# Optimization experiments

Measured on AMD Instinct MI355X. Metric: run time of the kernel, lower is better.

## Reference

```python
import jax, jax.numpy as jnp
import numpy as np
import math

B, S, D, H = 2, 2048, 1024, 16
DK = D // H
SCALE = math.sqrt(DK)
NEG_BIG = -1e9


def setup_inputs() -> dict:
    key = jax.random.key(0)
    ks = jax.random.split(key, 7)
    x = jax.random.normal(ks[0], (B, S, D), dtype=jnp.float32)
    # additive causal mask: 0 on/below diagonal, -inf above
    causal = jnp.triu(jnp.ones((S, S), dtype=bool), k=1)
    mask = jnp.where(causal, -jnp.inf, 0.0).astype(jnp.float32)
    key_padding_mask = jax.random.bernoulli(ks[1], 0.1, (B, S))
    init = 1.0 / math.sqrt(D)
    Wq = jax.random.normal(ks[2], (D, D), dtype=jnp.float32) * init
    Wk = jax.random.normal(ks[3], (D, D), dtype=jnp.float32) * init
    Wv = jax.random.normal(ks[4], (D, D), dtype=jnp.float32) * init
    Wo = jax.random.normal(ks[5], (D, D), dtype=jnp.float32) * init
    bo = jnp.zeros((D,), dtype=jnp.float32)
    return {"x": x, "mask": mask, "key_padding_mask": key_padding_mask,
            "Wq": Wq, "Wk": Wk, "Wv": Wv, "Wo": Wo, "bo": bo}


def reference(x, mask, key_padding_mask, Wq, Wk, Wv, Wo, bo):
    b, s, d = x.shape
    # project and split heads -> [B,H,S,Dk]
    def heads(W):
        return jnp.einsum('bsd,de->bse', x, W).reshape(b, s, H, DK).transpose(0, 2, 1, 3)
    Q, K, V = heads(Wq), heads(Wk), heads(Wv)
    scores = jnp.einsum('bhqd,bhkd->bhqk', Q, K) / SCALE          # [B,H,S,S]
    scores = scores + mask[None, None]                            # additive attn mask
    scores = jnp.where(key_padding_mask[:, None, None, :], -jnp.inf, scores)
    # rows whose max is -inf (fully masked) get all scores set to -1e9
    max_scores = jnp.max(scores, axis=-1, keepdims=True)
    scores = jnp.where(jnp.isinf(max_scores), NEG_BIG, scores)
    attn = jax.nn.softmax(scores, axis=-1)
    attn = jnp.where(jnp.isnan(attn), 0.0, attn)
    # dropout is identity in eval mode
    ctx = jnp.einsum('bhqk,bhkd->bhqd', attn, V)                  # [B,H,S,Dk]
    ctx = ctx.transpose(0, 2, 1, 3).reshape(b, s, d)
    return jnp.einsum('bsd,de->bse', ctx, Wo) + bo
```

## Files before the change

kernel.cpp:

```cpp
#include <hip/hip_runtime.h>
#include <stdint.h>

#define NB 2
#define NS 2048
#define ND 1024
#define NH 16
#define NDK 64

typedef __attribute__((ext_vector_type(8))) short s8v;
typedef __attribute__((ext_vector_type(4))) float f4v;
typedef __attribute__((ext_vector_type(4))) unsigned short us4v;
typedef __attribute__((ext_vector_type(8))) unsigned short us8v;
typedef __attribute__((ext_vector_type(2))) uint32_t u2v;

__device__ __forceinline__ unsigned short f2bf(float f) {
  uint32_t u = __builtin_bit_cast(uint32_t, f);
  u = (u + 0x7fffu + ((u >> 16) & 1u)) >> 16;
  return (unsigned short)u;
}
__device__ __forceinline__ float bf2f(unsigned short h) {
  uint32_t u = ((uint32_t)h) << 16;
  return __builtin_bit_cast(float, u);
}
__device__ __forceinline__ uint32_t cvtpk(float lo, float hi) {
  uint32_t r;
  asm("v_cvt_pk_bf16_f32 %0, %1, %2" : "=v"(r) : "v"(lo), "v"(hi));
  return r;
}

__device__ __forceinline__ void gload16(const void* g, void* l) {
  __builtin_amdgcn_global_load_lds(
      (const __attribute__((address_space(1))) void*)g,
      (__attribute__((address_space(3))) void*)l, 16, 0, 0);
}

__global__ void k_convert_x(const float* __restrict__ x, unsigned short* __restrict__ xbf) {
  int i = (blockIdx.x * 256 + threadIdx.x) * 4;
  float4 v = *(const float4*)(x + i);
  us4v o;
  o[0] = f2bf(v.x); o[1] = f2bf(v.y); o[2] = f2bf(v.z); o[3] = f2bf(v.w);
  *(us4v*)(xbf + i) = o;
}

__global__ void k_transpose_w(const float* __restrict__ Wq, const float* __restrict__ Wk,
                              const float* __restrict__ Wv, const float* __restrict__ Wo,
                              unsigned short* __restrict__ wt_qkv, unsigned short* __restrict__ wt_o) {
  __shared__ float tls[64][65];
  int bid = blockIdx.x;
  int mat = bid >> 8;
  int tile = bid & 255;
  int tk = tile >> 4, tn = tile & 15;
  const float* W = (mat == 0) ? Wq : (mat == 1) ? Wk : (mat == 2) ? Wv : Wo;
  int t = threadIdx.x;
  int lr = t >> 2;
  int lc0 = (t & 3) * 16;
  const float* src = W + (size_t)(tk * 64 + lr) * 1024 + tn * 64 + lc0;
#pragma unroll
  for (int j = 0; j < 16; j += 4) {
    float4 v = *(const float4*)(src + j);
    tls[lr][lc0 + j + 0] = v.x; tls[lr][lc0 + j + 1] = v.y;
    tls[lr][lc0 + j + 2] = v.z; tls[lr][lc0 + j + 3] = v.w;
  }
  __syncthreads();
  float scale = (mat == 0) ? 0.18033688f : 1.0f;
  int nr = t >> 2, kc0 = (t & 3) * 16;
  unsigned short* dst = ((mat < 3) ? (wt_qkv + (size_t)(mat * 1024 + tn * 64 + nr) * 1024)
                                   : (wt_o + (size_t)(tn * 64 + nr) * 1024)) + tk * 64 + kc0;
  us8v o0, o1;
#pragma unroll
  for (int j = 0; j < 8; j++) o0[j] = f2bf(tls[kc0 + j][nr] * scale);
#pragma unroll
  for (int j = 0; j < 8; j++) o1[j] = f2bf(tls[kc0 + 8 + j][nr] * scale);
  *(us8v*)(dst) = o0;
  *(us8v*)(dst + 8) = o1;
}

template <int MODE>
__global__ __launch_bounds__(256) void k_gemm(const unsigned short* __restrict__ A,
                                              const unsigned short* __restrict__ Bt,
                                              unsigned short* __restrict__ qklin,
                                              unsigned short* __restrict__ vt,
                                              const float* __restrict__ bias,
                                              float* __restrict__ out) {
  __shared__ unsigned short lds_a[2][128 * 32];
  __shared__ unsigned short lds_b[2][128 * 32];
  const int K = 1024;
  const int NT = K / 32;
  int bid = blockIdx.x;
  int xcd = bid & 7, local = bid >> 3;
  int m0 = (xcd * 4 + (local & 3)) * 128;
  int n0 = (local >> 2) * 128;
  int tid = threadIdx.x, lane = tid & 63, w = tid >> 6;
  int wm = w >> 1, wn = w & 1;
  int g = lane >> 4, c0 = lane & 15;
  int rrel = lane >> 2;
  int gran = lane & 3;
  int rsw = (rrel >> 1) & 3;
  int csw = (c0 >> 1) & 3;
  f4v acc[4][4];
#pragma unroll
  for (int mi = 0; mi < 4; mi++)
#pragma unroll
    for (int ni = 0; ni < 4; ni++) acc[mi][ni] = (f4v){0.f, 0.f, 0.f, 0.f};

#define STAGE(kt_, buf_)                                                        \
  do {                                                                          \
    int koff = (kt_)*32;                                                        \
    _Pragma("unroll") for (int i = 0; i < 2; i++) {                             \
      int r = 32 * w + 16 * i + rrel;                                           \
      gload16(A + (size_t)(m0 + r) * K + koff + 8 * (gran ^ rsw),               \
              (void*)(lds_a[buf_] + (32 * w + 16 * i) * 32));                   \
      gload16(Bt + (size_t)(n0 + r) * K + koff + 8 * (gran ^ rsw),              \
              (void*)(lds_b[buf_] + (32 * w + 16 * i) * 32));                   \
    }                                                                           \
  } while (0)

  STAGE(0, 0);
  __syncthreads();

  for (int kt = 0; kt < NT; ++kt) {
    int cur = kt & 1;
    if (kt + 1 < NT) STAGE(kt + 1, cur ^ 1);
    s8v af[4], bfr[4];
#pragma unroll
    for (int mi = 0; mi < 4; mi++) {
      int row = 64 * wm + 16 * mi + c0;
      af[mi] = *(const s8v*)(lds_a[cur] + row * 32 + 8 * (g ^ csw));
    }
#pragma unroll
    for (int ni = 0; ni < 4; ni++) {
      int row = 64 * wn + 16 * ni + c0;
      bfr[ni] = *(const s8v*)(lds_b[cur] + row * 32 + 8 * (g ^ csw));
    }
#pragma unroll
    for (int mi = 0; mi < 4; mi++)
#pragma unroll
      for (int ni = 0; ni < 4; ni++)
        acc[mi][ni] = __builtin_amdgcn_mfma_f32_16x16x32_bf16(af[mi], bfr[ni], acc[mi][ni], 0, 0, 0);
    __syncthreads();
  }
#undef STAGE

#pragma unroll
  for (int mi = 0; mi < 4; mi++)
#pragma unroll
    for (int ni = 0; ni < 4; ni++)
#pragma unroll
      for (int r = 0; r < 4; r++) {
        int m = m0 + 64 * wm + 16 * mi + 4 * g + r;
        int n = n0 + 64 * wn + 16 * ni + c0;
        float v = acc[mi][ni][r];
        if (MODE == 0) {
          unsigned short hv = f2bf(v);
          if (n < 2048) {
            qklin[(size_t)m * 2048 + n] = hv;
          } else {
            int b = m >> 11, s = m & 2047;
            int hh = (n - 2048) >> 6, dk = n & 63;
            vt[(size_t)((b * 16 + hh) * 64 + dk) * 2048 + s] = hv;
          }
        } else {
          out[(size_t)m * 1024 + n] = v + bias[n];
        }
      }
}

__global__ void k_vmean(const unsigned short* __restrict__ vt, float* __restrict__ vmean) {
  int row = blockIdx.x * 4 + (threadIdx.x >> 6);
  int lane = threadIdx.x & 63;
  const unsigned short* p = vt + (size_t)row * 2048 + lane * 32;
  float s = 0.f;
#pragma unroll
  for (int j = 0; j < 32; j += 8) {
    us8v v = *(const us8v*)(p + j);
#pragma unroll
    for (int e = 0; e < 8; e++) s += bf2f(v[e]);
  }
#pragma unroll
  for (int m = 1; m < 64; m <<= 1) s += __shfl_xor(s, m);
  if (lane == 0) vmean[row] = s * (1.0f / 2048.0f);
}

__global__ __launch_bounds__(256) void k_attn(const unsigned short* __restrict__ qklin,
                                              const unsigned short* __restrict__ vt,
                                              const int* __restrict__ kpm,
                                              const float* __restrict__ vmean,
                                              unsigned short* __restrict__ ctx) {
  __shared__ unsigned short lds_k[2][64 * 64];
  __shared__ unsigned short lds_v[2][64 * 64];
  __shared__ unsigned short p_lds[4][16 * 64];
  int wg = blockIdx.x;
  int w5 = wg >> 5, bh = wg & 31;
  int qt = (w5 < 8) ? 31 - w5 : (w5 < 16) ? w5 - 8 : (w5 < 24) ? 39 - w5 : w5 - 16;
  int b = bh >> 4, h = bh & 15;
  int tid = threadIdx.x, lane = tid & 63, w = tid >> 6;
  int g = lane >> 4, c0 = lane & 15;
  int q0 = qt * 64 + w * 16;
  unsigned short* pl = p_lds[w];
  int rrel = lane >> 3, gran = lane & 7;

  const unsigned short* ksrc0 = qklin + (size_t)(b * NS) * 2048 + 1024 + h * 64;
  const unsigned short* vsrc0 = vt + (size_t)(bh * 64) * 2048;

  const unsigned short* qbase = qklin + (size_t)(b * NS + q0 + c0) * 2048 + h * 64 + 8 * g;
  s8v qf0 = *(const s8v*)(qbase);
  s8v qf1 = *(const s8v*)(qbase + 32);

  f4v cacc[4];
#pragma unroll
  for (int d = 0; d < 4; d++) cacc[d] = (f4v){0.f, 0.f, 0.f, 0.f};
  float m_s = -1e30f, l_s = 0.f;
  int qrow = q0 + c0;

#define STAGEKV(it_, buf_)                                                      \
  do {                                                                          \
    int kb_ = (it_)*64;                                                         \
    _Pragma("unroll") for (int i = 0; i < 2; i++) {                             \
      int r = 16 * w + 8 * i + rrel;                                            \
      gload16(ksrc0 + (size_t)(kb_ + r) * 2048 + 8 * (gran ^ rrel),             \
              (void*)(lds_k[buf_] + (16 * w + 8 * i) * 64));                    \
      gload16(vsrc0 + (size_t)r * 2048 + kb_ + 8 * (gran ^ rrel),               \
              (void*)(lds_v[buf_] + (16 * w + 8 * i) * 64));                    \
    }                                                                           \
  } while (0)

  STAGEKV(0, 0);
  int kp_cur = kpm[b * NS + lane];

  int nkt = qt + 1;
  for (int it = 0; it < nkt; ++it) {
    int kb = it * 64;
    int cur = it & 1;
    int kp_next = 0;
    if (it + 1 < nkt) {
      STAGEKV(it + 1, cur ^ 1);
      kp_next = kpm[b * NS + (it + 1) * 64 + lane];
      asm volatile("s_waitcnt vmcnt(5)" ::: "memory");
    } else {
      asm volatile("s_waitcnt vmcnt(0)" ::: "memory");
    }
    __builtin_amdgcn_s_barrier();
    __builtin_amdgcn_sched_barrier(0);
    uint64_t padmask = __ballot(kp_cur != 0);
    f4v sacc[4];
#pragma unroll
    for (int t = 0; t < 4; t++) {
      int row = 16 * t + c0;
      s8v kf0 = *(const s8v*)(lds_k[cur] + row * 64 + 8 * (g ^ (c0 & 7)));
      s8v kf1 = *(const s8v*)(lds_k[cur] + row * 64 + 8 * ((4 + g) ^ (c0 & 7)));
      f4v z = (f4v){0.f, 0.f, 0.f, 0.f};
      z = __builtin_amdgcn_mfma_f32_16x16x32_bf16(kf0, qf0, z, 0, 0, 0);
      z = __builtin_amdgcn_mfma_f32_16x16x32_bf16(kf1, qf1, z, 0, 0, 0);
      sacc[t] = z;
    }
    int thr = qrow - kb;
    uint64_t cmask = (thr >= 63) ? ~0ull : ((2ull << thr) - 1ull);
    uint64_t valid = cmask & ~padmask;
    uint32_t vlo = (uint32_t)valid, vhi = (uint32_t)(valid >> 32);
    float p[4][4];
    float mx = -1e30f;
#pragma unroll
    for (int t = 0; t < 4; t++) {
      uint32_t half = (t & 2) ? vhi : vlo;
      uint32_t nib = (half >> (16 * (t & 1) + 4 * g)) & 0xFu;
#pragma unroll
      for (int r = 0; r < 4; r++) {
        float s = sacc[t][r];
        s = ((nib >> r) & 1u) ? s : -1e30f;
        p[t][r] = s;
      }
      mx = fmaxf(mx, fmaxf(fmaxf(p[t][0], p[t][1]), fmaxf(p[t][2], p[t][3])));
    }
    mx = fmaxf(mx, __shfl_xor(mx, 16));
    mx = fmaxf(mx, __shfl_xor(mx, 32));
    if (!__all(mx <= m_s + 11.0f)) {
      float mnew = fmaxf(m_s, mx);
      float a = __builtin_exp2f(m_s - mnew);
      m_s = mnew;
      l_s *= a;
      int ybase = 20 * g;
#pragma unroll
      for (int r = 0; r < 4; r++) {
        float ar = __shfl(a, ybase + r);
#pragma unroll
        for (int d = 0; d < 4; d++) cacc[d][r] *= ar;
      }
    }
    float rs = 0.f;
#pragma unroll
    for (int t = 0; t < 4; t++)
#pragma unroll
      for (int r = 0; r < 4; r++) {
        float e = __builtin_exp2f(p[t][r] - m_s);
        p[t][r] = e;
        rs += e;
      }
    rs += __shfl_xor(rs, 16);
    rs += __shfl_xor(rs, 32);
    rs = (m_s > -1e29f) ? rs : 0.f;
    l_s += rs;
#pragma unroll
    for (int t = 0; t < 4; t++) {
      u2v pk;
      pk[0] = cvtpk(p[t][0], p[t][1]);
      pk[1] = cvtpk(p[t][2], p[t][3]);
      int gr = (2 * t + (g >> 1)) ^ (c0 & 7);
      *(u2v*)((char*)pl + c0 * 128 + gr * 16 + 8 * (g & 1)) = pk;
    }
    asm volatile("s_waitcnt lgkmcnt(0)" ::: "memory");
    __builtin_amdgcn_sched_barrier(0);
#pragma unroll
    for (int c = 0; c < 2; c++) {
      int off = c0 * 128 + 16 * g + 64 * c;
      off ^= (c0 & 7) << 4;
      s8v pf = *(const s8v*)((const char*)pl + off);
#pragma unroll
      for (int d = 0; d < 4; d++) {
        int row = 16 * d + c0;
        s8v vf = *(const s8v*)(lds_v[cur] + row * 64 + 8 * ((4 * c + g) ^ (c0 & 7)));
        cacc[d] = __builtin_amdgcn_mfma_f32_16x16x32_bf16(pf, vf, cacc[d], 0, 0, 0);
      }
    }
    __builtin_amdgcn_s_barrier();
    __builtin_amdgcn_sched_barrier(0);
    kp_cur = kp_next;
  }
#undef STAGEKV
  float lq[4];
  {
    int ybase = 20 * g;
#pragma unroll
    for (int r = 0; r < 4; r++) lq[r] = __shfl(l_s, ybase + r);
  }
#pragma unroll
  for (int d = 0; d < 4; d++)
#pragma unroll
    for (int r = 0; r < 4; r++) {
      int q = q0 + 4 * g + r;
      float l = lq[r];
      float v = (l > 0.f) ? cacc[d][r] / l : vmean[bh * 64 + 16 * d + c0];
      ctx[(size_t)(b * NS + q) * ND + h * 64 + 16 * d + c0] = f2bf(v);
    }
}

extern "C" void kernel_launch(void* const* d_in, const int* in_sizes, int n_in,
                              void* d_out, int out_size, void* d_ws, size_t ws_size,
                              hipStream_t stream) {
  const float* x  = (const float*)d_in[0];
  const int* kpm  = (const int*)d_in[2];
  const float* Wq = (const float*)d_in[3];
  const float* Wk = (const float*)d_in[4];
  const float* Wv = (const float*)d_in[5];
  const float* Wo = (const float*)d_in[6];
  const float* bo = (const float*)d_in[7];

  char* ws = (char*)d_ws;
  unsigned short* xbf   = (unsigned short*)(ws);
  unsigned short* wtqkv = (unsigned short*)(ws + 8u * 1024 * 1024);
  unsigned short* wto   = (unsigned short*)(ws + 14u * 1024 * 1024);
  unsigned short* vt    = (unsigned short*)(ws + 16u * 1024 * 1024);
  float* vmean          = (float*)(ws + 24u * 1024 * 1024);
  unsigned short* ctx   = xbf;
  unsigned short* qklin = (unsigned short*)d_out;

  k_convert_x<<<4096, 256, 0, stream>>>(x, xbf);
  k_transpose_w<<<1024, 256, 0, stream>>>(Wq, Wk, Wv, Wo, wtqkv, wto);
  k_gemm<0><<<768, 256, 0, stream>>>(xbf, wtqkv, qklin, vt, nullptr, nullptr);
  k_vmean<<<512, 256, 0, stream>>>(vt, vmean);
  k_attn<<<1024, 256, 0, stream>>>(qklin, vt, kpm, vmean, ctx);
  k_gemm<1><<<256, 256, 0, stream>>>(ctx, wto, nullptr, nullptr, bo, (float*)d_out);
}
```

Measured before the change: 141.8 us.

## Switch attention to 32x32x16 MFMA with register-resident P via permlane32 swap

```diff
diff --git a/kernel.cpp b/kernel.cpp
--- a/kernel.cpp
+++ b/kernel.cpp
@@ -9,9 +9,10 @@
 
 typedef __attribute__((ext_vector_type(8))) short s8v;
 typedef __attribute__((ext_vector_type(4))) float f4v;
+typedef __attribute__((ext_vector_type(16))) float f16x;
 typedef __attribute__((ext_vector_type(4))) unsigned short us4v;
 typedef __attribute__((ext_vector_type(8))) unsigned short us8v;
-typedef __attribute__((ext_vector_type(2))) uint32_t u2v;
+typedef __attribute__((ext_vector_type(4))) uint32_t u4v;
 
 __device__ __forceinline__ unsigned short f2bf(float f) {
   uint32_t u = __builtin_bit_cast(uint32_t, f);
@@ -181,46 +182,49 @@
   if (lane == 0) vmean[row] = s * (1.0f / 2048.0f);
 }
 
-__global__ __launch_bounds__(256) void k_attn(const unsigned short* __restrict__ qklin,
+__global__ __launch_bounds__(128) void k_attn(const unsigned short* __restrict__ qklin,
                                               const unsigned short* __restrict__ vt,
                                               const int* __restrict__ kpm,
                                               const float* __restrict__ vmean,
                                               unsigned short* __restrict__ ctx) {
   __shared__ unsigned short lds_k[2][64 * 64];
   __shared__ unsigned short lds_v[2][64 * 64];
-  __shared__ unsigned short p_lds[4][16 * 64];
   int wg = blockIdx.x;
   int w5 = wg >> 5, bh = wg & 31;
   int qt = (w5 < 8) ? 31 - w5 : (w5 < 16) ? w5 - 8 : (w5 < 24) ? 39 - w5 : w5 - 16;
   int b = bh >> 4, h = bh & 15;
   int tid = threadIdx.x, lane = tid & 63, w = tid >> 6;
-  int g = lane >> 4, c0 = lane & 15;
-  int q0 = qt * 64 + w * 16;
-  unsigned short* pl = p_lds[w];
+  int l31 = lane & 31, hi = lane >> 5;
+  int q0 = qt * 64 + w * 32;
+  int qrow = q0 + l31;
   int rrel = lane >> 3, gran = lane & 7;
 
   const unsigned short* ksrc0 = qklin + (size_t)(b * NS) * 2048 + 1024 + h * 64;
   const unsigned short* vsrc0 = vt + (size_t)(bh * 64) * 2048;
 
-  const unsigned short* qbase = qklin + (size_t)(b * NS + q0 + c0) * 2048 + h * 64 + 8 * g;
-  s8v qf0 = *(const s8v*)(qbase);
-  s8v qf1 = *(const s8v*)(qbase + 32);
-
-  f4v cacc[4];
-#pragma unroll
-  for (int d = 0; d < 4; d++) cacc[d] = (f4v){0.f, 0.f, 0.f, 0.f};
+  s8v qf[4];
+  {
+    const unsigned short* qb = qklin + (size_t)(b * NS + qrow) * 2048 + h * 64 + 8 * hi;
+#pragma unroll
+    for (int dd = 0; dd < 4; dd++) qf[dd] = *(const s8v*)(qb + 16 * dd);
+  }
+
+  f16x oacc[2];
+#pragma unroll
+  for (int db = 0; db < 2; db++)
+#pragma unroll
+    for (int r = 0; r < 16; r++) oacc[db][r] = 0.f;
   float m_s = -1e30f, l_s = 0.f;
-  int qrow = q0 + c0;
 
 #define STAGEKV(it_, buf_)                                                      \
   do {                                                                          \
     int kb_ = (it_)*64;                                                         \
-    _Pragma("unroll") for (int i = 0; i < 2; i++) {                             \
-      int r = 16 * w + 8 * i + rrel;                                            \
+    _Pragma("unroll") for (int i = 0; i < 4; i++) {                             \
+      int r = 16 * i + 8 * w + rrel;                                            \
       gload16(ksrc0 + (size_t)(kb_ + r) * 2048 + 8 * (gran ^ rrel),             \
-              (void*)(lds_k[buf_] + (16 * w + 8 * i) * 64));                    \
+              (void*)(lds_k[buf_] + (16 * i + 8 * w) * 64));                    \
       gload16(vsrc0 + (size_t)r * 2048 + kb_ + 8 * (gran ^ rrel),               \
-              (void*)(lds_v[buf_] + (16 * w + 8 * i) * 64));                    \
+              (void*)(lds_v[buf_] + (16 * i + 8 * w) * 64));                    \
     }                                                                           \
   } while (0)
 
@@ -235,111 +239,108 @@
     if (it + 1 < nkt) {
       STAGEKV(it + 1, cur ^ 1);
       kp_next = kpm[b * NS + (it + 1) * 64 + lane];
-      asm volatile("s_waitcnt vmcnt(5)" ::: "memory");
+      asm volatile("s_waitcnt vmcnt(9)" ::: "memory");
     } else {
       asm volatile("s_waitcnt vmcnt(0)" ::: "memory");
     }
     __builtin_amdgcn_s_barrier();
     __builtin_amdgcn_sched_barrier(0);
     uint64_t padmask = __ballot(kp_cur != 0);
-    f4v sacc[4];
-#pragma unroll
-    for (int t = 0; t < 4; t++) {
-      int row = 16 * t + c0;
-      s8v kf0 = *(const s8v*)(lds_k[cur] + row * 64 + 8 * (g ^ (c0 & 7)));
-      s8v kf1 = *(const s8v*)(lds_k[cur] + row * 64 + 8 * ((4 + g) ^ (c0 & 7)));
-      f4v z = (f4v){0.f, 0.f, 0.f, 0.f};
-      z = __builtin_amdgcn_mfma_f32_16x16x32_bf16(kf0, qf0, z, 0, 0, 0);
-      z = __builtin_amdgcn_mfma_f32_16x16x32_bf16(kf1, qf1, z, 0, 0, 0);
-      sacc[t] = z;
+    f16x sa[2];
+#pragma unroll
+    for (int kb2 = 0; kb2 < 2; kb2++) {
+      f16x z;
+#pragma unroll
+      for (int r = 0; r < 16; r++) z[r] = 0.f;
+#pragma unroll
+      for (int dd = 0; dd < 4; dd++) {
+        s8v kf = *(const s8v*)(lds_k[cur] + (32 * kb2 + l31) * 64 +
+                               8 * ((2 * dd + hi) ^ (l31 & 7)));
+        z = __builtin_amdgcn_mfma_f32_32x32x16_bf16(kf, qf[dd], z, 0, 0, 0);
+      }
+      sa[kb2] = z;
     }
     int thr = qrow - kb;
     uint64_t cmask = (thr >= 63) ? ~0ull : ((2ull << thr) - 1ull);
     uint64_t valid = cmask & ~padmask;
-    uint32_t vlo = (uint32_t)valid, vhi = (uint32_t)(valid >> 32);
-    float p[4][4];
+    uint32_t vw0 = ((uint32_t)valid) >> (4 * hi);
+    uint32_t vw1 = ((uint32_t)(valid >> 32)) >> (4 * hi);
     float mx = -1e30f;
 #pragma unroll
-    for (int t = 0; t < 4; t++) {
-      uint32_t half = (t & 2) ? vhi : vlo;
-      uint32_t nib = (half >> (16 * (t & 1) + 4 * g)) & 0xFu;
-#pragma unroll
-      for (int r = 0; r < 4; r++) {
-        float s = sacc[t][r];
-        s = ((nib >> r) & 1u) ? s : -1e30f;
-        p[t][r] = s;
-      }
-      mx = fmaxf(mx, fmaxf(fmaxf(p[t][0], p[t][1]), fmaxf(p[t][2], p[t][3])));
-    }
-    mx = fmaxf(mx, __shfl_xor(mx, 16));
+    for (int kb2 = 0; kb2 < 2; kb2++) {
+      uint32_t vw = kb2 ? vw1 : vw0;
+#pragma unroll
+      for (int r = 0; r < 16; r++) {
+        float s = sa[kb2][r];
+        s = ((vw >> ((r & 3) + 8 * (r >> 2))) & 1u) ? s : -1e30f;
+        sa[kb2][r] = s;
+        mx = fmaxf(mx, s);
+      }
+    }
     mx = fmaxf(mx, __shfl_xor(mx, 32));
     if (!__all(mx <= m_s + 11.0f)) {
       float mnew = fmaxf(m_s, mx);
       float a = __builtin_exp2f(m_s - mnew);
       m_s = mnew;
       l_s *= a;
-      int ybase = 20 * g;
-#pragma unroll
-      for (int r = 0; r < 4; r++) {
-        float ar = __shfl(a, ybase + r);
-#pragma unroll
-        for (int d = 0; d < 4; d++) cacc[d][r] *= ar;
+#pragma unroll
+      for (int r = 0; r < 16; r++) {
+        float ar = __shfl(a, (r & 3) + 8 * (r >> 2) + 4 * hi);
+        oacc[0][r] *= ar;
+        oacc[1][r] *= ar;
       }
     }
     float rs = 0.f;
 #pragma unroll
-    for (int t = 0; t < 4; t++)
-#pragma unroll
-      for (int r = 0; r < 4; r++) {
-        float e = __builtin_exp2f(p[t][r] - m_s);
-        p[t][r] = e;
+    for (int kb2 = 0; kb2 < 2; kb2++)
+#pragma unroll
+      for (int r = 0; r < 16; r++) {
+        float e = __builtin_exp2f(sa[kb2][r] - m_s);
+        sa[kb2][r] = e;
         rs += e;
       }
-    rs += __shfl_xor(rs, 16);
     rs += __shfl_xor(rs, 32);
     rs = (m_s > -1e29f) ? rs : 0.f;
     l_s += rs;
-#pragma unroll
-    for (int t = 0; t < 4; t++) {
-      u2v pk;
-      pk[0] = cvtpk(p[t][0], p[t][1]);
-      pk[1] = cvtpk(p[t][2], p[t][3]);
-      int gr = (2 * t + (g >> 1)) ^ (c0 & 7);
-      *(u2v*)((char*)pl + c0 * 128 + gr * 16 + 8 * (g & 1)) = pk;
-    }
-    asm volatile("s_waitcnt lgkmcnt(0)" ::: "memory");
-    __builtin_amdgcn_sched_barrier(0);
-#pragma unroll
-    for (int c = 0; c < 2; c++) {
-      int off = c0 * 128 + 16 * g + 64 * c;
-      off ^= (c0 & 7) << 4;
-      s8v pf = *(const s8v*)((const char*)pl + off);
-#pragma unroll
-      for (int d = 0; d < 4; d++) {
-        int row = 16 * d + c0;
-        s8v vf = *(const s8v*)(lds_v[cur] + row * 64 + 8 * ((4 * c + g) ^ (c0 & 7)));
-        cacc[d] = __builtin_amdgcn_mfma_f32_16x16x32_bf16(pf, vf, cacc[d], 0, 0, 0);
-      }
-    }
+    s8v pa[4];
+#pragma unroll
+    for (int kb2 = 0; kb2 < 2; kb2++)
+#pragma unroll
+      for (int c = 0; c < 2; c++) {
+        uint32_t A0 = cvtpk(sa[kb2][8 * c + 0], sa[kb2][8 * c + 1]);
+        uint32_t B0 = cvtpk(sa[kb2][8 * c + 4], sa[kb2][8 * c + 5]);
+        uint32_t A1 = cvtpk(sa[kb2][8 * c + 2], sa[kb2][8 * c + 3]);
+        uint32_t B1 = cvtpk(sa[kb2][8 * c + 6], sa[kb2][8 * c + 7]);
+        asm("v_permlane32_swap_b32 %0, %1" : "+v"(A0), "+v"(B0));
+        asm("v_permlane32_swap_b32 %0, %1" : "+v"(A1), "+v"(B1));
+        u4v t = {A0, A1, B0, B1};
+        pa[2 * kb2 + c] = __builtin_bit_cast(s8v, t);
+      }
+#pragma unroll
+    for (int db = 0; db < 2; db++)
+#pragma unroll
+      for (int kk = 0; kk < 4; kk++) {
+        s8v vf = *(const s8v*)(lds_v[cur] + (32 * db + l31) * 64 +
+                               8 * ((2 * kk + hi) ^ (l31 & 7)));
+        oacc[db] = __builtin_amdgcn_mfma_f32_32x32x16_bf16(pa[kk], vf, oacc[db], 0, 0, 0);
+      }
     __builtin_amdgcn_s_barrier();
     __builtin_amdgcn_sched_barrier(0);
     kp_cur = kp_next;
   }
 #undef STAGEKV
-  float lq[4];
-  {
-    int ybase = 20 * g;
-#pragma unroll
-    for (int r = 0; r < 4; r++) lq[r] = __shfl(l_s, ybase + r);
-  }
-#pragma unroll
-  for (int d = 0; d < 4; d++)
-#pragma unroll
-    for (int r = 0; r < 4; r++) {
-      int q = q0 + 4 * g + r;
+  float lq[16];
+#pragma unroll
+  for (int r = 0; r < 16; r++) lq[r] = __shfl(l_s, (r & 3) + 8 * (r >> 2) + 4 * hi);
+#pragma unroll
+  for (int db = 0; db < 2; db++)
+#pragma unroll
+    for (int r = 0; r < 16; r++) {
+      int q = q0 + (r & 3) + 8 * (r >> 2) + 4 * hi;
+      int d = 32 * db + l31;
       float l = lq[r];
-      float v = (l > 0.f) ? cacc[d][r] / l : vmean[bh * 64 + 16 * d + c0];
-      ctx[(size_t)(b * NS + q) * ND + h * 64 + 16 * d + c0] = f2bf(v);
+      float v = (l > 0.f) ? oacc[db][r] / l : vmean[bh * 64 + d];
+      ctx[(size_t)(b * NS + q) * ND + h * 64 + d] = f2bf(v);
     }
 }
 
@@ -367,6 +368,6 @@
   k_transpose_w<<<1024, 256, 0, stream>>>(Wq, Wk, Wv, Wo, wtqkv, wto);
   k_gemm<0><<<768, 256, 0, stream>>>(xbf, wtqkv, qklin, vt, nullptr, nullptr);
   k_vmean<<<512, 256, 0, stream>>>(vt, vmean);
-  k_attn<<<1024, 256, 0, stream>>>(qklin, vt, kpm, vmean, ctx);
+  k_attn<<<1024, 128, 0, stream>>>(qklin, vt, kpm, vmean, ctx);
   k_gemm<1><<<256, 256, 0, stream>>>(ctx, wto, nullptr, nullptr, bo, (float*)d_out);
 }
```

Measured after the change: 158.8 us. +12.0%, slower.
